# Performance work log

Measured on AMD Instinct MI355X. Metric: run time of the kernel, lower is better.

## Reference

```python
import jax, jax.numpy as jnp
import numpy as np

KS = 5  # kernel_size


def _conv(x, w, b):
    # valid cross-correlation, same math as unfold + w.view matmul + fold
    y = jax.lax.conv_general_dilated(
        x, w, window_strides=(1, 1), padding='VALID',
        dimension_numbers=('NCHW', 'OIHW', 'NCHW'))
    return y + b


def _avgpool2(x):
    # non-overlapping 2x2 average pool (unfold(2,2,stride=2) + mean over patch)
    B, C, H, W = x.shape
    return x.reshape(B, C, H // 2, 2, W // 2, 2).mean(axis=(3, 5))


def setup_inputs() -> dict:
    key = jax.random.key(0)
    ks = jax.random.split(key, 8)
    h1, h2 = 10, 20
    L1n, L2n, L3n, out_n = 4 * 4 * h2, 120, 84, 10

    def xavier(k, shape, fan_in, fan_out):
        std = np.sqrt(2.0 / (fan_in + fan_out))
        return jax.random.normal(k, shape, dtype=jnp.float32) * std

    x = jax.random.normal(ks[0], (8192, 1, 28, 28), dtype=jnp.float32)
    W1 = xavier(ks[1], (h1, 1, KS, KS), 1 * KS * KS, h1 * KS * KS)
    b1 = jnp.zeros((1, h1, 1, 1), jnp.float32)
    W2 = xavier(ks[2], (h2, h1, KS, KS), h1 * KS * KS, h2 * KS * KS)
    b2 = jnp.zeros((1, h2, 1, 1), jnp.float32)
    L1 = jax.random.normal(ks[3], (L1n, L2n), dtype=jnp.float32)
    Lb1 = jnp.zeros((1, L2n), jnp.float32)
    L2 = jax.random.normal(ks[4], (L2n, L3n), dtype=jnp.float32)
    Lb2 = jnp.zeros((1, L3n), jnp.float32)
    L3 = jax.random.normal(ks[5], (L3n, out_n), dtype=jnp.float32)
    Lb3 = jnp.zeros((1, out_n), jnp.float32)
    return {'x': x, 'W1': W1, 'b1': b1, 'W2': W2, 'b2': b2,
            'L1': L1, 'Lb1': Lb1, 'L2': L2, 'Lb2': Lb2, 'L3': L3, 'Lb3': Lb3}


def reference(x, W1, b1, W2, b2, L1, Lb1, L2, Lb2, L3, Lb3):
    h = jax.nn.sigmoid(_avgpool2(_conv(x, W1, b1)))      # [B,10,12,12]
    h = jax.nn.sigmoid(_avgpool2(_conv(h, W2, b2)))      # [B,20,4,4]
    h = h.reshape(h.shape[0], -1)                        # [B,320]
    h = jax.nn.sigmoid(h @ L1 + Lb1)                     # [B,120]
    h = jax.nn.sigmoid(h @ L2 + Lb2)                     # [B,84]
    return h @ L3 + Lb3                                  # [B,10]
```

## Files before the change

kernel.cpp:

```cpp
#include <hip/hip_runtime.h>
#include <hip/hip_fp16.h>
#include <math.h>


__device__ __forceinline__ float sigf(float v) {
    return 1.0f / (1.0f + __expf(-v));
}

__global__ void k_prep(const float* __restrict__ W1, const float* __restrict__ W2,
                       float* __restrict__ w6, float* __restrict__ w2q) {
    int i = blockIdx.x * 256 + threadIdx.x;
    if (i < 5000) {
        int kx = i % 5, t = i / 5;
        int ky = t % 5, t2 = t / 5;
        int ic = t2 % 10, c = t2 / 10;
        w2q[((ic * 5 + ky) * 20 + c) * 5 + kx] = W2[i];
    }
    int k = i - 5000;
    if (k >= 0 && k < 480) {
        int kx = k % 8, t = k / 8;
        int c = t % 10, ky = t / 10;
        float v = 0.f;
        if (kx < 6) {
            for (int dy = 0; dy < 2; ++dy)
                for (int dx = 0; dx < 2; ++dx) {
                    int sy = ky - dy, sx = kx - dx;
                    if (sy >= 0 && sy < 5 && sx >= 0 && sx < 5)
                        v += W1[c * 25 + sy * 5 + sx];
                }
        }
        w6[k] = v;
    }
}

#define S1IM 1328

__global__ __launch_bounds__(512) void k_conv1(
    const float* __restrict__ x, const float* __restrict__ w6g,
    const float* __restrict__ b1, __half* __restrict__ S1h) {
    __shared__ float4 XR[4 * 224];
    __shared__ float wq1[480];
    __shared__ float bs1[10];

    const int tid = threadIdx.x;
    const long img0 = (long)blockIdx.x * 4;

    {
        const float4* xg = (const float4*)(x + img0 * 784);
        for (int i = tid; i < 784; i += 512) {
            int im = i / 196, j = i % 196, r = j / 7, kk = j % 7;
            XR[im * 224 + r * 8 + (kk ^ ((r >> 1) & 7))] = xg[i];
        }
    }
    if (tid < 480) wq1[tid] = w6g[tid];
    else if (tid < 490) bs1[tid - 480] = b1[tid - 480];
    __syncthreads();

    const int w = tid >> 6, l = tid & 63;
    const int im = w >> 1, chbase = (w & 1) * 5;
    const long img = img0 + im;
    if (l < 60) {
        const int c = l / 12, py = l % 12;
        const int ch = chbase + c;
        float acc[12];
#pragma unroll
        for (int p = 0; p < 12; ++p) acc[p] = 0.f;

        const float4* xr = &XR[im * 224];
#pragma unroll
        for (int ky = 0; ky < 6; ++ky) {
            const int r = 2 * py + ky;
            const int hsh = (r >> 1) & 7;
            const int base = r * 8;
            union { float4 v[7]; float f[28]; } R;
#pragma unroll
            for (int q = 0; q < 7; ++q) R.v[q] = xr[base + (q ^ hsh)];
            union { float4 v[2]; float f[8]; } W;
            const float* wb = &wq1[(ky * 10 + ch) * 8];
            W.v[0] = *(const float4*)(wb);
            W.v[1] = *(const float4*)(wb + 4);
#pragma unroll
            for (int kx = 0; kx < 6; ++kx) {
                const float wv = W.f[kx];
#pragma unroll
                for (int px = 0; px < 12; ++px)
                    acc[px] += R.f[2 * px + kx] * wv;
            }
        }

        float h[12];
#pragma unroll
        for (int px = 0; px < 12; ++px)
            h[px] = sigf(acc[px] * 0.25f + bs1[ch]);
        float hh[11];
#pragma unroll
        for (int t = 0; t < 11; ++t) hh[t] = h[t] + h[t + 1];
        float o[12];
#pragma unroll
        for (int t = 0; t < 11; ++t)
            o[t] = hh[t] + __shfl_down(hh[t], 1, 64);
        o[11] = 0.f;
        if (py < 11) {
            union { __half hs[12]; uint2 u2[3]; } P;
#pragma unroll
            for (int t = 0; t < 12; ++t) P.hs[t] = __float2half(o[t]);
            __half* sp = S1h + img * S1IM + ch * 132 + py * 12;
            ((uint2*)sp)[0] = P.u2[0];
            ((uint2*)sp)[1] = P.u2[1];
            ((uint2*)sp)[2] = P.u2[2];
        }
    }
}

__global__ __launch_bounds__(320) void k_conv2(
    const __half* __restrict__ S1h, const float* __restrict__ w2qg,
    const float* __restrict__ b2, float* __restrict__ h2) {
    const int w = threadIdx.x >> 6, l = threadIdx.x & 63;
    const int cg = __builtin_amdgcn_readfirstlane(w);
    const int im = l >> 3, py = (l >> 1) & 3, xh = l & 1;
    const int grp = gridDim.x / 8;
    const int bidr = ((grp - 1 - ((int)blockIdx.x >> 3)) << 3) | ((int)blockIdx.x & 7);
    const long img0 = (long)bidr * 8;

    float acc[4][2];
#pragma unroll
    for (int a = 0; a < 4; ++a) { acc[a][0] = 0.f; acc[a][1] = 0.f; }

    const __half* s1 = S1h + (img0 + im) * S1IM;
    const float* wg = w2qg + cg * 20;
    for (int ic = 0; ic < 10; ++ic) {
#pragma unroll
        for (int ky = 0; ky < 5; ++ky) {
            const __half* rp = s1 + ic * 132 + (2 * py + ky) * 12 + xh * 4;
            union { uint2 u; __half2 h2v[2]; } A, B;
            A.u = *(const uint2*)(rp);
            B.u = *(const uint2*)(rp + 4);
            union { float4 v[2]; float f[8]; } R;
            float2 f0 = __half22float2(A.h2v[0]);
            float2 f1 = __half22float2(A.h2v[1]);
            float2 f2 = __half22float2(B.h2v[0]);
            float2 f3 = __half22float2(B.h2v[1]);
            R.f[0] = f0.x; R.f[1] = f0.y; R.f[2] = f1.x; R.f[3] = f1.y;
            R.f[4] = f2.x; R.f[5] = f2.y; R.f[6] = f3.x; R.f[7] = f3.y;
            const float* wrow = wg + (ic * 5 + ky) * 100;
#pragma unroll
            for (int cc = 0; cc < 4; ++cc)
#pragma unroll
                for (int kx = 0; kx < 5; ++kx) {
                    const float wv = wrow[cc * 5 + kx];
                    acc[cc][0] += R.f[kx] * wv;
                    acc[cc][1] += R.f[2 + kx] * wv;
                }
        }
    }

    float* outp = h2 + (img0 + im) * 320 + (cg * 4) * 16 + py * 4 + xh * 2;
#pragma unroll
    for (int cc = 0; cc < 4; ++cc) {
        const float bv = b2[cg * 4 + cc];
        float2 o;
        o.x = sigf(acc[cc][0] * 0.25f + bv);
        o.y = sigf(acc[cc][1] * 0.25f + bv);
        *(float2*)(outp + cc * 16) = o;
    }
}

#define TSTR 18
__global__ __launch_bounds__(256) void k_fc(
    const float* __restrict__ h2, const float* __restrict__ L1,
    const float* __restrict__ Lb1, const float* __restrict__ L2,
    const float* __restrict__ Lb2, const float* __restrict__ L3,
    const float* __restrict__ Lb3, float* __restrict__ out) {
    __shared__ float arena[18480];
    float* h2t = arena;
    float* wt  = arena + 5760;
    float* g1t = arena + 13952;
    float* g2t = arena + 16112;
    float* L3s = arena + 17624;

    const int tid = threadIdx.x;
    const long img0 = (long)blockIdx.x * 16;

    for (int i = tid; i < 1280; i += 256) {
        const int im = i / 80, fq = i % 80;
        float4 v = *(const float4*)(h2 + (img0 + im) * 320 + fq * 4);
        h2t[(fq * 4 + 0) * TSTR + im] = v.x;
        h2t[(fq * 4 + 1) * TSTR + im] = v.y;
        h2t[(fq * 4 + 2) * TSTR + im] = v.z;
        h2t[(fq * 4 + 3) * TSTR + im] = v.w;
    }
#pragma unroll
    for (int r = 0; r < 4; ++r) {
        const int idx = tid + 256 * r, row = idx >> 5, c4 = idx & 31;
        if (c4 < 30)
            *(float4*)(wt + row * 128 + c4 * 4) =
                *(const float4*)(L1 + row * 120 + c4 * 4);
    }
    __syncthreads();

    const int p = tid >> 5, jg = tid & 31;
    const int jc = jg < 30 ? jg : 29;

    float acc[4][2];
    {
        union { float4 v; float f[4]; } bv;
        bv.v = *(const float4*)(Lb1 + jc * 4);
#pragma unroll
        for (int q = 0; q < 4; ++q) { acc[q][0] = bv.f[q]; acc[q][1] = bv.f[q]; }
    }
    int cur = 0;
    for (int t = 0; t < 10; ++t) {
        float4 wr0, wr1, wr2, wr3;
        if (t < 9) {
            const int k0n = (t + 1) * 32;
            const int c0 = tid & 31;
            wr0 = (c0 < 30) ? *(const float4*)(L1 + (k0n + (tid >> 5)) * 120 + c0 * 4) : make_float4(0, 0, 0, 0);
            wr1 = (c0 < 30) ? *(const float4*)(L1 + (k0n + ((tid + 256) >> 5)) * 120 + c0 * 4) : make_float4(0, 0, 0, 0);
            wr2 = (c0 < 30) ? *(const float4*)(L1 + (k0n + ((tid + 512) >> 5)) * 120 + c0 * 4) : make_float4(0, 0, 0, 0);
            wr3 = (c0 < 30) ? *(const float4*)(L1 + (k0n + ((tid + 768) >> 5)) * 120 + c0 * 4) : make_float4(0, 0, 0, 0);
        }
        const float* wb = wt + cur * 4096;
        const int kb = t * 32;
#pragma unroll
        for (int k = 0; k < 32; ++k) {
            union { float4 v; float f[4]; } w;
            w.v = *(const float4*)(wb + k * 128 + jc * 4);
            const float2 h = *(const float2*)&h2t[(kb + k) * TSTR + p * 2];
#pragma unroll
            for (int q = 0; q < 4; ++q) {
                acc[q][0] += w.f[q] * h.x;
                acc[q][1] += w.f[q] * h.y;
            }
        }
        if (t < 9) {
            float* wd = wt + (cur ^ 1) * 4096;
            const int c0 = tid & 31;
            if (c0 < 30) {
                *(float4*)(wd + (tid >> 5) * 128 + c0 * 4) = wr0;
                *(float4*)(wd + ((tid + 256) >> 5) * 128 + c0 * 4) = wr1;
                *(float4*)(wd + ((tid + 512) >> 5) * 128 + c0 * 4) = wr2;
                *(float4*)(wd + ((tid + 768) >> 5) * 128 + c0 * 4) = wr3;
            }
            cur ^= 1;
        }
        __syncthreads();
    }
    if (jg < 30) {
#pragma unroll
        for (int q = 0; q < 4; ++q) {
            g1t[(jg * 4 + q) * TSTR + p * 2 + 0] = sigf(acc[q][0]);
            g1t[(jg * 4 + q) * TSTR + p * 2 + 1] = sigf(acc[q][1]);
        }
    }
    __syncthreads();

    for (int i = tid; i < 2520; i += 256) {
        const int row = i / 21, c4 = i % 21;
        *(float4*)(arena + row * 88 + c4 * 4) =
            *(const float4*)(L2 + row * 84 + c4 * 4);
    }
    for (int i = tid; i < 840; i += 256) L3s[i] = L3[i];
    if (tid < 10) L3s[840 + tid] = Lb3[tid];
    __syncthreads();

    if (jg < 21) {
        union { float4 v; float f[4]; } bv;
        bv.v = *(const float4*)(Lb2 + jg * 4);
        float a2[4][2];
#pragma unroll
        for (int q = 0; q < 4; ++q) { a2[q][0] = bv.f[q]; a2[q][1] = bv.f[q]; }
#pragma unroll 4
        for (int k = 0; k < 120; ++k) {
            union { float4 v; float f[4]; } w;
            w.v = *(const float4*)(arena + k * 88 + jg * 4);
            const float2 h = *(const float2*)&g1t[k * TSTR + p * 2];
#pragma unroll
            for (int q = 0; q < 4; ++q) {
                a2[q][0] += w.f[q] * h.x;
                a2[q][1] += w.f[q] * h.y;
            }
        }
#pragma unroll
        for (int q = 0; q < 4; ++q) {
            g2t[(jg * 4 + q) * TSTR + p * 2 + 0] = sigf(a2[q][0]);
            g2t[(jg * 4 + q) * TSTR + p * 2 + 1] = sigf(a2[q][1]);
        }
    }
    __syncthreads();

    if (tid < 160) {
        const int im = tid / 10, j = tid % 10;
        float a = L3s[840 + j];
#pragma unroll 4
        for (int i = 0; i < 84; ++i)
            a += g2t[i * TSTR + im] * L3s[i * 10 + j];
        out[(img0 + im) * 10 + j] = a;
    }
}

extern "C" void kernel_launch(void* const* d_in, const int* in_sizes, int n_in,
                              void* d_out, int out_size, void* d_ws, size_t ws_size,
                              hipStream_t stream) {
    const float* x   = (const float*)d_in[0];
    const float* W1  = (const float*)d_in[1];
    const float* b1  = (const float*)d_in[2];
    const float* W2  = (const float*)d_in[3];
    const float* b2  = (const float*)d_in[4];
    const float* L1  = (const float*)d_in[5];
    const float* Lb1 = (const float*)d_in[6];
    const float* L2  = (const float*)d_in[7];
    const float* Lb2 = (const float*)d_in[8];
    const float* L3  = (const float*)d_in[9];
    const float* Lb3 = (const float*)d_in[10];
    float* out = (float*)d_out;

    const int B = in_sizes[0] / 784;

    char* ws = (char*)d_ws;
    float* w6   = (float*)ws;
    float* w2q  = (float*)(ws + 4096);
    __half* S1h = (__half*)(ws + 4096 + 32768);
    float* h2   = (float*)(ws + 4096 + 32768 + (size_t)B * S1IM * 2);

    hipLaunchKernelGGL(k_prep, dim3(22), dim3(256), 0, stream, W1, W2, w6, w2q);
    hipLaunchKernelGGL(k_conv1, dim3(B / 4), dim3(512), 0, stream, x, w6, b1, S1h);
    hipLaunchKernelGGL(k_conv2, dim3(B / 8), dim3(320), 0, stream, S1h, w2q, b2, h2);
    hipLaunchKernelGGL(k_fc, dim3(B / 16), dim3(256), 0, stream,
                       h2, L1, Lb1, L2, Lb2, L3, Lb3, out);
}
```

Before: 83.35 us.

## Fuse conv2 stage into fully-connected kernel, computing features directly into shared memory

Removes the separate conv2 kernel and computes the second convolution, pooling and sigmoid inside the fc kernel, writing results straight into the transposed shared-memory tile. This eliminates the global write and read of the intermediate h2 buffer and one kernel launch. In exchange, conv2 work now runs with the fc kernel's block shape, with a partly idle final loop iteration and a different lane-to-image mapping that may coalesce loads less well.

```diff
diff --git a/kernel.cpp b/kernel.cpp
--- a/kernel.cpp
+++ b/kernel.cpp
@@ -112,62 +112,10 @@
     }
 }
 
-__global__ __launch_bounds__(320) void k_conv2(
-    const __half* __restrict__ S1h, const float* __restrict__ w2qg,
-    const float* __restrict__ b2, float* __restrict__ h2) {
-    const int w = threadIdx.x >> 6, l = threadIdx.x & 63;
-    const int cg = __builtin_amdgcn_readfirstlane(w);
-    const int im = l >> 3, py = (l >> 1) & 3, xh = l & 1;
-    const int grp = gridDim.x / 8;
-    const int bidr = ((grp - 1 - ((int)blockIdx.x >> 3)) << 3) | ((int)blockIdx.x & 7);
-    const long img0 = (long)bidr * 8;
-
-    float acc[4][2];
-#pragma unroll
-    for (int a = 0; a < 4; ++a) { acc[a][0] = 0.f; acc[a][1] = 0.f; }
-
-    const __half* s1 = S1h + (img0 + im) * S1IM;
-    const float* wg = w2qg + cg * 20;
-    for (int ic = 0; ic < 10; ++ic) {
-#pragma unroll
-        for (int ky = 0; ky < 5; ++ky) {
-            const __half* rp = s1 + ic * 132 + (2 * py + ky) * 12 + xh * 4;
-            union { uint2 u; __half2 h2v[2]; } A, B;
-            A.u = *(const uint2*)(rp);
-            B.u = *(const uint2*)(rp + 4);
-            union { float4 v[2]; float f[8]; } R;
-            float2 f0 = __half22float2(A.h2v[0]);
-            float2 f1 = __half22float2(A.h2v[1]);
-            float2 f2 = __half22float2(B.h2v[0]);
-            float2 f3 = __half22float2(B.h2v[1]);
-            R.f[0] = f0.x; R.f[1] = f0.y; R.f[2] = f1.x; R.f[3] = f1.y;
-            R.f[4] = f2.x; R.f[5] = f2.y; R.f[6] = f3.x; R.f[7] = f3.y;
-            const float* wrow = wg + (ic * 5 + ky) * 100;
-#pragma unroll
-            for (int cc = 0; cc < 4; ++cc)
-#pragma unroll
-                for (int kx = 0; kx < 5; ++kx) {
-                    const float wv = wrow[cc * 5 + kx];
-                    acc[cc][0] += R.f[kx] * wv;
-                    acc[cc][1] += R.f[2 + kx] * wv;
-                }
-        }
-    }
-
-    float* outp = h2 + (img0 + im) * 320 + (cg * 4) * 16 + py * 4 + xh * 2;
-#pragma unroll
-    for (int cc = 0; cc < 4; ++cc) {
-        const float bv = b2[cg * 4 + cc];
-        float2 o;
-        o.x = sigf(acc[cc][0] * 0.25f + bv);
-        o.y = sigf(acc[cc][1] * 0.25f + bv);
-        *(float2*)(outp + cc * 16) = o;
-    }
-}
-
 #define TSTR 18
 __global__ __launch_bounds__(256) void k_fc(
-    const float* __restrict__ h2, const float* __restrict__ L1,
+    const __half* __restrict__ S1h, const float* __restrict__ w2qg,
+    const float* __restrict__ b2, const float* __restrict__ L1,
     const float* __restrict__ Lb1, const float* __restrict__ L2,
     const float* __restrict__ Lb2, const float* __restrict__ L3,
     const float* __restrict__ Lb3, float* __restrict__ out) {
@@ -181,14 +129,52 @@
     const int tid = threadIdx.x;
     const long img0 = (long)blockIdx.x * 16;
 
-    for (int i = tid; i < 1280; i += 256) {
-        const int im = i / 80, fq = i % 80;
-        float4 v = *(const float4*)(h2 + (img0 + im) * 320 + fq * 4);
-        h2t[(fq * 4 + 0) * TSTR + im] = v.x;
-        h2t[(fq * 4 + 1) * TSTR + im] = v.y;
-        h2t[(fq * 4 + 2) * TSTR + im] = v.z;
-        h2t[(fq * 4 + 3) * TSTR + im] = v.w;
-    }
+    for (int u = tid; u < 640; u += 256) {
+        const int im = u & 15, r = u >> 4;
+        const int cg = __builtin_amdgcn_readfirstlane(r / 8);
+        const int py = (r >> 1) & 3, xh = r & 1;
+
+        float acc[4][2];
+#pragma unroll
+        for (int a = 0; a < 4; ++a) { acc[a][0] = 0.f; acc[a][1] = 0.f; }
+
+        const __half* s1 = S1h + (img0 + im) * S1IM;
+        const float* wg = w2qg + cg * 20;
+        for (int ic = 0; ic < 10; ++ic) {
+#pragma unroll
+            for (int ky = 0; ky < 5; ++ky) {
+                const __half* rp = s1 + ic * 132 + (2 * py + ky) * 12 + xh * 4;
+                union { uint2 u2; __half2 h2v[2]; } A, Bv;
+                A.u2 = *(const uint2*)(rp);
+                Bv.u2 = *(const uint2*)(rp + 4);
+                float R[8];
+                float2 f0 = __half22float2(A.h2v[0]);
+                float2 f1 = __half22float2(A.h2v[1]);
+                float2 f2 = __half22float2(Bv.h2v[0]);
+                float2 f3 = __half22float2(Bv.h2v[1]);
+                R[0] = f0.x; R[1] = f0.y; R[2] = f1.x; R[3] = f1.y;
+                R[4] = f2.x; R[5] = f2.y; R[6] = f3.x; R[7] = f3.y;
+                const float* wrow = wg + (ic * 5 + ky) * 100;
+#pragma unroll
+                for (int cc = 0; cc < 4; ++cc)
+#pragma unroll
+                    for (int kx = 0; kx < 5; ++kx) {
+                        const float wv = wrow[cc * 5 + kx];
+                        acc[cc][0] += R[kx] * wv;
+                        acc[cc][1] += R[2 + kx] * wv;
+                    }
+            }
+        }
+
+#pragma unroll
+        for (int cc = 0; cc < 4; ++cc) {
+            const float bv = b2[cg * 4 + cc];
+            const int feat = (cg * 4 + cc) * 16 + py * 4 + xh * 2;
+            h2t[feat * TSTR + im] = sigf(acc[cc][0] * 0.25f + bv);
+            h2t[(feat + 1) * TSTR + im] = sigf(acc[cc][1] * 0.25f + bv);
+        }
+    }
+
 #pragma unroll
     for (int r = 0; r < 4; ++r) {
         const int idx = tid + 256 * r, row = idx >> 5, c4 = idx & 31;
@@ -254,9 +240,10 @@
     }
     __syncthreads();
 
+    float* w2s = arena;
     for (int i = tid; i < 2520; i += 256) {
         const int row = i / 21, c4 = i % 21;
-        *(float4*)(arena + row * 88 + c4 * 4) =
+        *(float4*)(w2s + row * 88 + c4 * 4) =
             *(const float4*)(L2 + row * 84 + c4 * 4);
     }
     for (int i = tid; i < 840; i += 256) L3s[i] = L3[i];
@@ -272,7 +259,7 @@
 #pragma unroll 4
         for (int k = 0; k < 120; ++k) {
             union { float4 v; float f[4]; } w;
-            w.v = *(const float4*)(arena + k * 88 + jg * 4);
+            w.v = *(const float4*)(w2s + k * 88 + jg * 4);
             const float2 h = *(const float2*)&g1t[k * TSTR + p * 2];
 #pragma unroll
             for (int q = 0; q < 4; ++q) {
@@ -320,11 +307,9 @@
     float* w6   = (float*)ws;
     float* w2q  = (float*)(ws + 4096);
     __half* S1h = (__half*)(ws + 4096 + 32768);
-    float* h2   = (float*)(ws + 4096 + 32768 + (size_t)B * S1IM * 2);
 
     hipLaunchKernelGGL(k_prep, dim3(22), dim3(256), 0, stream, W1, W2, w6, w2q);
     hipLaunchKernelGGL(k_conv1, dim3(B / 4), dim3(512), 0, stream, x, w6, b1, S1h);
-    hipLaunchKernelGGL(k_conv2, dim3(B / 8), dim3(320), 0, stream, S1h, w2q, b2, h2);
     hipLaunchKernelGGL(k_fc, dim3(B / 16), dim3(256), 0, stream,
-                       h2, L1, Lb1, L2, Lb2, L3, Lb3, out);
-}
+                       S1h, w2q, b2, L1, Lb1, L2, Lb2, L3, Lb3, out);
+}
```

After: 87.57 us. +5.1%, slower.
